# Kernel tuning notes

Hardware: AMD Instinct MI355X
Metric: run time of the kernel (lower is better)

Reference implementation:

```python
import jax, jax.numpy as jnp
import numpy as np

B, D, N, H = 4, 1024, 2048, 16
HD = D // H  # head dim = 64


def rotate_half(x):
    # pairs (x1, x2) -> (-x2, x1), interleaved along last dim
    x1 = x[..., 0::2]
    x2 = x[..., 1::2]
    return jnp.stack((-x2, x1), axis=-1).reshape(x.shape)


def apply_cached_rotary_emb(freqs, t):
    return t * freqs[0] + rotate_half(t) * freqs[1]


def setup_inputs() -> dict:
    key = jax.random.key(0)
    ks = jax.random.split(key, 13)
    s = 1.0 / np.sqrt(D)
    inp = {
        "query": jax.random.normal(ks[0], (B, D, N), jnp.float32),
        "key": jax.random.normal(ks[1], (B, D, N), jnp.float32),
        "value": jax.random.normal(ks[2], (B, D, N), jnp.float32),
        "encoding": jax.random.normal(ks[3], (2, 1, 1, N, HD), jnp.float32),
        "Wq": jax.random.normal(ks[4], (D, D), jnp.float32) * s,
        "bq": jax.random.normal(ks[5], (D,), jnp.float32) * s,
        "Wk": jax.random.normal(ks[6], (D, D), jnp.float32) * s,
        "bk": jax.random.normal(ks[7], (D,), jnp.float32) * s,
        "Wv": jax.random.normal(ks[8], (D, D), jnp.float32) * s,
        "bv": jax.random.normal(ks[9], (D,), jnp.float32) * s,
        "Wm": jax.random.normal(ks[10], (D, D), jnp.float32) * s,
        "bm": jax.random.normal(ks[11], (D,), jnp.float32) * s,
    }
    return inp


def reference(query, key, value, encoding, Wq, bq, Wk, bk, Wv, bv, Wm, bm):
    b, d_model, n = query.shape

    def proj(W, bias, x):  # Conv1d with kernel_size=1 == pointwise matmul
        return jnp.einsum('oi,bin->bon', W, x) + bias[None, :, None]

    # [B, D, N] -> [B, HD, H, N]  (channel split: dim-major, as in .view(B, dim, H, -1))
    q = proj(Wq, bq, query).reshape(b, HD, H, n)
    k = proj(Wk, bk, key).reshape(b, HD, H, n)
    v = proj(Wv, bv, value).reshape(b, HD, H, n)

    # RoPE applied in [B, H, N, HD] layout, then back to [B, HD, H, N]
    q = jnp.transpose(apply_cached_rotary_emb(encoding, jnp.transpose(q, (0, 2, 3, 1))), (0, 3, 1, 2))
    k = jnp.transpose(apply_cached_rotary_emb(encoding, jnp.transpose(k, (0, 2, 3, 1))), (0, 3, 1, 2))

    scores = jnp.einsum('bdhn,bdhm->bhnm', q, k) / np.float32(np.sqrt(HD))
    prob = jax.nn.softmax(scores, axis=-1)
    x = jnp.einsum('bhnm,bdhm->bdhn', prob, v)

    out = jnp.einsum('oi,bin->bon', Wm, x.reshape(b, d_model, n)) + bm[None, :, None]
    return out
```

## Files before the change

### kernel.cpp

```cpp
#include <hip/hip_runtime.h>
#include <hip/hip_bf16.h>

typedef __bf16 bf16;
typedef __bf16 bf16x8 __attribute__((ext_vector_type(8)));
typedef __bf16 bf16x4 __attribute__((ext_vector_type(4)));
typedef float f32x4 __attribute__((ext_vector_type(4)));
typedef unsigned int uint4v __attribute__((ext_vector_type(4)));
typedef unsigned int uint2v __attribute__((ext_vector_type(2)));

#define LOG2E 1.44269504088896340736f

typedef __attribute__((address_space(1))) const unsigned int guint;
typedef __attribute__((address_space(3))) unsigned int luint;

__device__ __forceinline__ void gload_lds16(const bf16* g, bf16* l) {
  __builtin_amdgcn_global_load_lds((guint*)g, (luint*)l, 16, 0, 0);
}

__global__ __launch_bounds__(256) void k_transpose3(const float* __restrict__ q,
                                                    const float* __restrict__ k,
                                                    const float* __restrict__ v,
                                                    bf16* __restrict__ tq,
                                                    bf16* __restrict__ tk,
                                                    bf16* __restrict__ tv) {
  __shared__ bf16 T[64][72];
  const int t = threadIdx.x;
  const int n0 = blockIdx.x * 64;
  const int i0 = blockIdx.y * 64;
  const int z = blockIdx.z;
  const int b = z & 3, which = z >> 2;
  const float* src = (which == 0) ? q : ((which == 1) ? k : v);
  bf16* dst = (which == 0) ? tq : ((which == 1) ? tk : tv);
  const size_t srcb = (size_t)b * 1024 * 2048;
#pragma unroll
  for (int p = 0; p < 2; ++p) {
    int idx = p * 256 + t;
    int row = idx >> 3;
    int seg = idx & 7;
    const float* sp = src + srcb + (size_t)(i0 + row) * 2048 + n0 + seg * 8;
    f32x4 a = *(const f32x4*)sp;
    f32x4 c = *(const f32x4*)(sp + 4);
    bf16x8 o;
#pragma unroll
    for (int e = 0; e < 4; ++e) { o[e] = (bf16)a[e]; o[4 + e] = (bf16)c[e]; }
    *(bf16x8*)&T[row][seg * 8] = o;
  }
  __syncthreads();
  const int j = t >> 2;
  const int iseg = t & 3;
  bf16x8 o0, o1;
#pragma unroll
  for (int e = 0; e < 8; ++e) o0[e] = T[iseg * 16 + e][j];
#pragma unroll
  for (int e = 0; e < 8; ++e) o1[e] = T[iseg * 16 + 8 + e][j];
  bf16* dp = dst + (size_t)b * 2048 * 1024 + (size_t)(n0 + j) * 1024 + i0 + iseg * 16;
  *(bf16x8*)dp = o0;
  *(bf16x8*)(dp + 8) = o1;
}

__global__ __launch_bounds__(256) void k_gemm3(const bf16* __restrict__ Wqb,
                                               const bf16* __restrict__ Wkb,
                                               const bf16* __restrict__ Wvb,
                                               const float* __restrict__ bq,
                                               const float* __restrict__ bk,
                                               const float* __restrict__ bv,
                                               const bf16* __restrict__ tq,
                                               const bf16* __restrict__ tk,
                                               const bf16* __restrict__ tv,
                                               bf16* __restrict__ qp,
                                               bf16* __restrict__ kp,
                                               bf16* __restrict__ vp) {
  const int K = 1024, Nn = 2048;
  const int z = blockIdx.z;
  const int b = z & 3, which = z >> 2;
  const bf16* A = (which == 0) ? Wqb : ((which == 1) ? Wkb : Wvb);
  const bf16* Bt = (which == 0) ? tq : ((which == 1) ? tk : tv);
  const float* bias = (which == 0) ? bq : ((which == 1) ? bk : bv);
  bf16* C = (which == 0) ? qp : ((which == 1) ? kp : vp);

  __shared__ bf16 As[128 * 32];
  __shared__ bf16 Bs[128 * 32];
  const int t = threadIdx.x;
  const int w = t >> 6, l = t & 63, q = l >> 4, li = l & 15;
  const int o0 = blockIdx.y * 128, n0 = blockIdx.x * 128;
  const bf16* Ab = A + (size_t)o0 * K;
  const bf16* Bb = Bt + (size_t)b * Nn * K + (size_t)n0 * K;
  const int wr = (w >> 1) * 64, wc = (w & 1) * 64;
  f32x4 acc[4][4];
#pragma unroll
  for (int i = 0; i < 4; ++i)
#pragma unroll
    for (int j = 0; j < 4; ++j) acc[i][j] = (f32x4){0.f, 0.f, 0.f, 0.f};

  const int sidx0 = w * 64 + l;
  const int srow0 = sidx0 >> 2, sseg0 = (sidx0 & 3) * 8;
  const int sidx1 = 256 + sidx0;
  const int srow1 = sidx1 >> 2, sseg1 = (sidx1 & 3) * 8;
  bf16* ldsA0 = As + (size_t)(w * 64) * 8;
  bf16* ldsA1 = As + (size_t)(256 + w * 64) * 8;
  bf16* ldsB0 = Bs + (size_t)(w * 64) * 8;
  bf16* ldsB1 = Bs + (size_t)(256 + w * 64) * 8;

  for (int k0 = 0; k0 < K; k0 += 32) {
    __syncthreads();
    gload_lds16(Ab + (size_t)srow0 * K + k0 + sseg0, ldsA0);
    gload_lds16(Ab + (size_t)srow1 * K + k0 + sseg1, ldsA1);
    gload_lds16(Bb + (size_t)srow0 * K + k0 + sseg0, ldsB0);
    gload_lds16(Bb + (size_t)srow1 * K + k0 + sseg1, ldsB1);
    __syncthreads();
    bf16x8 af[4], bfr[4];
#pragma unroll
    for (int mt = 0; mt < 4; ++mt) af[mt] = *(const bf16x8*)&As[(wr + mt * 16 + li) * 32 + q * 8];
#pragma unroll
    for (int c = 0; c < 4; ++c) bfr[c] = *(const bf16x8*)&Bs[(wc + c * 16 + li) * 32 + q * 8];
#pragma unroll
    for (int mt = 0; mt < 4; ++mt)
#pragma unroll
      for (int c = 0; c < 4; ++c)
        acc[mt][c] = __builtin_amdgcn_mfma_f32_16x16x32_bf16(af[mt], bfr[c], acc[mt][c], 0, 0, 0);
  }

  bf16* Cb = C + (size_t)b * K * Nn;
#pragma unroll
  for (int mt = 0; mt < 4; ++mt) {
#pragma unroll
    for (int r = 0; r < 4; ++r) {
      int o = o0 + wr + mt * 16 + q * 4 + r;
      float bvv = bias[o];
#pragma unroll
      for (int c = 0; c < 4; ++c) {
        int n = n0 + wc + c * 16 + li;
        Cb[(size_t)o * Nn + n] = (bf16)(acc[mt][c][r] + bvv);
      }
    }
  }
}

template <typename OT>
__global__ __launch_bounds__(256) void k_gemm(const bf16* __restrict__ A,
                                              const bf16* __restrict__ Bt,
                                              const float* __restrict__ bias,
                                              OT* __restrict__ C,
                                              int M, int K, int Nn) {
  __shared__ bf16 As[128 * 32];
  __shared__ bf16 Bs[128 * 32];
  const int t = threadIdx.x;
  const int w = t >> 6, l = t & 63, q = l >> 4, li = l & 15;
  const int o0 = blockIdx.y * 128, n0 = blockIdx.x * 128;
  const int b = blockIdx.z;
  const bf16* Ab = A + (size_t)o0 * K;
  const bf16* Bb = Bt + (size_t)b * Nn * K + (size_t)n0 * K;
  const int wr = (w >> 1) * 64, wc = (w & 1) * 64;
  f32x4 acc[4][4];
#pragma unroll
  for (int i = 0; i < 4; ++i)
#pragma unroll
    for (int j = 0; j < 4; ++j) acc[i][j] = (f32x4){0.f, 0.f, 0.f, 0.f};

  const int sidx0 = w * 64 + l;
  const int srow0 = sidx0 >> 2, sseg0 = (sidx0 & 3) * 8;
  const int sidx1 = 256 + sidx0;
  const int srow1 = sidx1 >> 2, sseg1 = (sidx1 & 3) * 8;
  bf16* ldsA0 = As + (size_t)(w * 64) * 8;
  bf16* ldsA1 = As + (size_t)(256 + w * 64) * 8;
  bf16* ldsB0 = Bs + (size_t)(w * 64) * 8;
  bf16* ldsB1 = Bs + (size_t)(256 + w * 64) * 8;

  for (int k0 = 0; k0 < K; k0 += 32) {
    __syncthreads();
    gload_lds16(Ab + (size_t)srow0 * K + k0 + sseg0, ldsA0);
    gload_lds16(Ab + (size_t)srow1 * K + k0 + sseg1, ldsA1);
    gload_lds16(Bb + (size_t)srow0 * K + k0 + sseg0, ldsB0);
    gload_lds16(Bb + (size_t)srow1 * K + k0 + sseg1, ldsB1);
    __syncthreads();
    bf16x8 af[4], bfr[4];
#pragma unroll
    for (int mt = 0; mt < 4; ++mt) af[mt] = *(const bf16x8*)&As[(wr + mt * 16 + li) * 32 + q * 8];
#pragma unroll
    for (int c = 0; c < 4; ++c) bfr[c] = *(const bf16x8*)&Bs[(wc + c * 16 + li) * 32 + q * 8];
#pragma unroll
    for (int mt = 0; mt < 4; ++mt)
#pragma unroll
      for (int c = 0; c < 4; ++c)
        acc[mt][c] = __builtin_amdgcn_mfma_f32_16x16x32_bf16(af[mt], bfr[c], acc[mt][c], 0, 0, 0);
  }

  OT* Cb = C + (size_t)b * M * Nn;
#pragma unroll
  for (int mt = 0; mt < 4; ++mt) {
#pragma unroll
    for (int r = 0; r < 4; ++r) {
      int o = o0 + wr + mt * 16 + q * 4 + r;
      float bv = bias[o];
#pragma unroll
      for (int c = 0; c < 4; ++c) {
        int n = n0 + wc + c * 16 + li;
        Cb[(size_t)o * Nn + n] = (OT)(acc[mt][c][r] + bv);
      }
    }
  }
}

__global__ __launch_bounds__(256) void k_rope2(const bf16* __restrict__ qp,
                                               const bf16* __restrict__ kp,
                                               const float* __restrict__ enc,
                                               bf16* __restrict__ qa,
                                               bf16* __restrict__ ka) {
  __shared__ bf16 T[64][72];
  const int t = threadIdx.x;
  const int n0 = blockIdx.x * 64;
  const int h = blockIdx.y;
  const int z = blockIdx.z;
  const int b = z & 3, which = z >> 2;
  const bf16* src = which ? kp : qp;
  bf16* dst = which ? ka : qa;
  const float oscale = which ? 1.0f : 0.125f * LOG2E;
#pragma unroll
  for (int p = 0; p < 2; ++p) {
    int idx = p * 256 + t;
    int hd = idx >> 3;
    int seg = idx & 7;
    *(bf16x8*)&T[hd][seg * 8] =
        *(const bf16x8*)(src + (size_t)(b * 1024 + hd * 16 + h) * 2048 + n0 + seg * 8);
  }
  __syncthreads();
  const int j = t >> 2;
  const int hd0 = (t & 3) * 16;
  const int n = n0 + j;
  const float* e0 = enc + (size_t)n * 64 + hd0;
  const float* e1 = enc + (size_t)2048 * 64 + (size_t)n * 64 + hd0;
  bf16x8 o0, o1;
#pragma unroll
  for (int i = 0; i < 8; ++i) {
    int e = 2 * i;
    float t0 = (float)T[hd0 + e][j];
    float t1 = (float)T[hd0 + e + 1][j];
    float f00 = e0[e], f01 = e0[e + 1];
    float f10 = e1[e], f11 = e1[e + 1];
    float r0 = (t0 * f00 - t1 * f10) * oscale;
    float r1 = (t1 * f01 + t0 * f11) * oscale;
    if (i < 4) { o0[e & 7] = (bf16)r0; o0[(e & 7) + 1] = (bf16)r1; }
    else       { o1[e & 7] = (bf16)r0; o1[(e & 7) + 1] = (bf16)r1; }
  }
  bf16* dp = dst + ((size_t)(b * 16 + h) * 2048 + n) * 64 + hd0;
  *(bf16x8*)dp = o0;
  *(bf16x8*)(dp + 8) = o1;
}

__global__ __launch_bounds__(256, 4) void k_attn(const bf16* __restrict__ qa,
                                                 const bf16* __restrict__ ka,
                                                 const bf16* __restrict__ vp,
                                                 bf16* __restrict__ xo) {
  __shared__ bf16 Ks[64 * 72];
  __shared__ bf16 Vs[64 * 72];
  const int t = threadIdx.x;
  const int w = t >> 6, l = t & 63, q = l >> 4, li = l & 15;
  const int n0 = blockIdx.x * 128, h = blockIdx.y, b = blockIdx.z;
  const bool oddrow = ((t >> 4) & 1) != 0;
  const bf16* Qb = qa + (size_t)(b * 16 + h) * 2048 * 64;
  const bf16* Kb = ka + (size_t)(b * 16 + h) * 2048 * 64;
  const bf16* Vb = vp + (size_t)b * 1024 * 2048 + (size_t)h * 2048;

  const int r0 = t >> 3, s0 = (t & 7) * 8;
  const int r1 = (256 + t) >> 3, s1 = (t & 7) * 8;

  bf16x8 qf[2][2];
#pragma unroll
  for (int bt = 0; bt < 2; ++bt)
#pragma unroll
    for (int kk = 0; kk < 2; ++kk)
      qf[bt][kk] = *(const bf16x8*)(Qb + (size_t)(n0 + w * 32 + bt * 16 + li) * 64 + kk * 32 + q * 8);

  bf16x8 onef;
#pragma unroll
  for (int e = 0; e < 8; ++e) onef[e] = (bf16)1.0f;

  f32x4 acc[4][2];
#pragma unroll
  for (int i = 0; i < 4; ++i)
#pragma unroll
    for (int j = 0; j < 2; ++j) acc[i][j] = (f32x4){0.f, 0.f, 0.f, 0.f};
  f32x4 accl[2] = {(f32x4){0.f, 0.f, 0.f, 0.f}, (f32x4){0.f, 0.f, 0.f, 0.f}};

  bf16x8 kr0, kr1, vr0, vr1;
  kr0 = *(const bf16x8*)(Kb + (size_t)r0 * 64 + s0);
  kr1 = *(const bf16x8*)(Kb + (size_t)r1 * 64 + s1);
  vr0 = *(const bf16x8*)(Vb + (size_t)r0 * 32768 + s0);
  vr1 = *(const bf16x8*)(Vb + (size_t)r1 * 32768 + s1);
  *(bf16x8*)&Ks[r0 * 72 + s0] = kr0;
  *(bf16x8*)&Ks[r1 * 72 + s1] = kr1;
  *(bf16x8*)&Vs[r0 * 72 + s0] = vr0;
  *(bf16x8*)&Vs[r1 * 72 + s1] = vr1;
  __syncthreads();

  for (int m0 = 0; m0 < 2048; m0 += 64) {
    const int mn = (m0 + 64 < 2048) ? m0 + 64 : m0;
    kr0 = *(const bf16x8*)(Kb + (size_t)(mn + r0) * 64 + s0);
    kr1 = *(const bf16x8*)(Kb + (size_t)(mn + r1) * 64 + s1);
    vr0 = *(const bf16x8*)(Vb + (size_t)r0 * 32768 + mn + s0);
    vr1 = *(const bf16x8*)(Vb + (size_t)r1 * 32768 + mn + s1);

    f32x4 sacc[4][2];
#pragma unroll
    for (int mt = 0; mt < 4; ++mt)
#pragma unroll
      for (int bt = 0; bt < 2; ++bt) sacc[mt][bt] = (f32x4){0.f, 0.f, 0.f, 0.f};
#pragma unroll
    for (int kk = 0; kk < 2; ++kk) {
#pragma unroll
      for (int mt = 0; mt < 4; ++mt) {
        bf16x8 af = *(const bf16x8*)&Ks[(mt * 16 + li) * 72 + kk * 32 + q * 8];
#pragma unroll
        for (int bt = 0; bt < 2; ++bt)
          sacc[mt][bt] = __builtin_amdgcn_mfma_f32_16x16x32_bf16(af, qf[bt][kk], sacc[mt][bt], 0, 0, 0);
      }
    }

    unsigned pk32[2][4][2];
#pragma unroll
    for (int mt = 0; mt < 4; ++mt)
#pragma unroll
      for (int bt = 0; bt < 2; ++bt) {
        bf16x4 pk;
#pragma unroll
        for (int r = 0; r < 4; ++r) pk[r] = (bf16)__builtin_amdgcn_exp2f(sacc[mt][bt][r]);
        uint2v pu = __builtin_bit_cast(uint2v, pk);
        pk32[bt][mt][0] = pu[0];
        pk32[bt][mt][1] = pu[1];
      }

#pragma unroll
    for (int kk = 0; kk < 2; ++kk) {
      bf16x8 pf[2];
#pragma unroll
      for (int bt = 0; bt < 2; ++bt) {
        uint4v du;
#pragma unroll
        for (int hh = 0; hh < 2; ++hh) {
          unsigned p0 = pk32[bt][2 * kk + 0][hh];
          unsigned p1 = pk32[bt][2 * kk + 1][hh];
          uint2v ab = __builtin_amdgcn_permlane32_swap(p0, p1, false, false);
          unsigned A = ab[0];
          unsigned Bv = ab[1];
          unsigned swzA = (unsigned)__builtin_amdgcn_ds_swizzle((int)A, 0x401F);
          unsigned swzB = (unsigned)__builtin_amdgcn_ds_swizzle((int)Bv, 0x401F);
          du[hh]     = oddrow ? swzB : A;
          du[2 + hh] = oddrow ? Bv : swzA;
        }
        pf[bt] = __builtin_bit_cast(bf16x8, du);
        accl[bt] = __builtin_amdgcn_mfma_f32_16x16x32_bf16(onef, pf[bt], accl[bt], 0, 0, 0);
      }
#pragma unroll
      for (int hdt = 0; hdt < 4; ++hdt) {
        bf16x8 vf = *(const bf16x8*)&Vs[(hdt * 16 + li) * 72 + kk * 32 + q * 8];
#pragma unroll
        for (int bt = 0; bt < 2; ++bt)
          acc[hdt][bt] = __builtin_amdgcn_mfma_f32_16x16x32_bf16(vf, pf[bt], acc[hdt][bt], 0, 0, 0);
      }
    }

    __syncthreads();
    *(bf16x8*)&Ks[r0 * 72 + s0] = kr0;
    *(bf16x8*)&Ks[r1 * 72 + s1] = kr1;
    *(bf16x8*)&Vs[r0 * 72 + s0] = vr0;
    *(bf16x8*)&Vs[r1 * 72 + s1] = vr1;
    __syncthreads();
  }

  float inv[2] = {1.0f / accl[0][0], 1.0f / accl[1][0]};

  bf16* xb = xo + (size_t)b * 2048 * 1024 + (size_t)h * 64;
#pragma unroll
  for (int hdt = 0; hdt < 4; ++hdt)
#pragma unroll
    for (int bt = 0; bt < 2; ++bt) {
      int n = n0 + w * 32 + bt * 16 + li;
      bf16x4 o;
#pragma unroll
      for (int r = 0; r < 4; ++r) o[r] = (bf16)(acc[hdt][bt][r] * inv[bt]);
      *(bf16x4*)(xb + (size_t)n * 1024 + hdt * 16 + q * 4) = o;
    }
}

__global__ __launch_bounds__(256) void k_prepw(const float* __restrict__ Wq,
                                               const float* __restrict__ Wk,
                                               const float* __restrict__ Wv,
                                               const float* __restrict__ Wm,
                                               bf16* __restrict__ oq,
                                               bf16* __restrict__ ok,
                                               bf16* __restrict__ ov,
                                               bf16* __restrict__ om) {
  const int which = blockIdx.y;
  if (which < 3) {
    const float* s = (which == 0) ? Wq : ((which == 1) ? Wk : Wv);
    bf16* d = (which == 0) ? oq : ((which == 1) ? ok : ov);
    int idx = (blockIdx.x * 256 + threadIdx.x) * 4;
    f32x4 a = *(const f32x4*)(s + idx);
    bf16x4 o;
#pragma unroll
    for (int e = 0; e < 4; ++e) o[e] = (bf16)a[e];
    *(bf16x4*)(d + idx) = o;
  } else {
#pragma unroll
    for (int p = 0; p < 4; ++p) {
      int idx = (blockIdx.x * 4 + p) * 256 + threadIdx.x;
      int o = idx >> 10, j = idx & 1023;
      int hd = j & 63, hh = j >> 6;
      om[idx] = (bf16)Wm[((size_t)o << 10) + (size_t)(hd * 16 + hh)];
    }
  }
}

extern "C" void kernel_launch(void* const* d_in, const int* in_sizes, int n_in,
                              void* d_out, int out_size, void* d_ws, size_t ws_size,
                              hipStream_t stream) {
  const float* query = (const float*)d_in[0];
  const float* key   = (const float*)d_in[1];
  const float* value = (const float*)d_in[2];
  const float* enc   = (const float*)d_in[3];
  const float* Wq = (const float*)d_in[4];  const float* bq = (const float*)d_in[5];
  const float* Wk = (const float*)d_in[6];  const float* bk = (const float*)d_in[7];
  const float* Wv = (const float*)d_in[8];  const float* bv = (const float*)d_in[9];
  const float* Wm = (const float*)d_in[10]; const float* bm = (const float*)d_in[11];

  char* ws = (char*)d_ws;
  const size_t SZ = (size_t)4 * 2048 * 1024 * 2;
  const size_t WZ = (size_t)1024 * 1024 * 2;
  bf16* bufA = (bf16*)(ws + 0 * SZ);
  bf16* bufB = (bf16*)(ws + 1 * SZ);
  bf16* bufC = (bf16*)(ws + 2 * SZ);
  bf16* bufD = (bf16*)(ws + 3 * SZ);
  bf16* Wqb  = (bf16*)(ws + 4 * SZ + 0 * WZ);
  bf16* Wkb  = (bf16*)(ws + 4 * SZ + 1 * WZ);
  bf16* Wvb  = (bf16*)(ws + 4 * SZ + 2 * WZ);
  bf16* Wmp  = (bf16*)(ws + 4 * SZ + 3 * WZ);
  bf16* vt   = (bf16*)d_out;
  bf16* vpd  = (bf16*)d_out + (size_t)4 * 2048 * 1024;

  dim3 blk(256);
  k_prepw<<<dim3(1024, 4), blk, 0, stream>>>(Wq, Wk, Wv, Wm, Wqb, Wkb, Wvb, Wmp);
  k_transpose3<<<dim3(32, 16, 12), blk, 0, stream>>>(query, key, value, bufA, bufB, vt);
  k_gemm3<<<dim3(16, 8, 12), blk, 0, stream>>>(Wqb, Wkb, Wvb, bq, bk, bv,
                                               bufA, bufB, vt, bufC, bufD, vpd);
  k_rope2<<<dim3(32, 16, 8), blk, 0, stream>>>(bufC, bufD, enc, bufA, bufB);
  k_attn<<<dim3(16, 16, 4), blk, 0, stream>>>(bufA, bufB, vpd, bufC);
  k_gemm<float><<<dim3(16, 8, 4), blk, 0, stream>>>(Wmp, bufC, bm, (float*)d_out, 1024, 1024, 2048);
}
```

Before: 362.3 us.

## Double-buffer K/V LDS tiles in attention and remap block order for XCD locality

The attention kernel now keeps two LDS buffers for the K and V tiles. The next tile is written into the idle buffer, so each iteration needs one barrier instead of two. All three GEMM/attention kernels also remap the linear block index so that consecutive blocks that share operands land on the same XCD (dsp&7 chiplet interleave), which should improve L2 reuse. Doubling LDS raises per-block shared memory to about 36KB. That could limit occupancy under the 4-blocks-per-CU launch bound.

New measurement: 375.3 us. 1.04x slower.

```diff
diff --git a/kernel.cpp b/kernel.cpp
--- a/kernel.cpp
+++ b/kernel.cpp
@@ -71,8 +71,10 @@
                                                bf16* __restrict__ kp,
                                                bf16* __restrict__ vp) {
   const int K = 1024, Nn = 2048;
-  const int z = blockIdx.z;
-  const int b = z & 3, which = z >> 2;
+  const int dsp = blockIdx.x + 16 * (blockIdx.y + 8 * blockIdx.z);
+  const int wfi = (dsp & 7) * 192 + (dsp >> 3);
+  const int bx = wfi & 15, by = (wfi >> 4) & 7, bz = wfi >> 7;
+  const int b = bz & 3, which = bz >> 2;
   const bf16* A = (which == 0) ? Wqb : ((which == 1) ? Wkb : Wvb);
   const bf16* Bt = (which == 0) ? tq : ((which == 1) ? tk : tv);
   const float* bias = (which == 0) ? bq : ((which == 1) ? bk : bv);
@@ -82,7 +84,7 @@
   __shared__ bf16 Bs[128 * 32];
   const int t = threadIdx.x;
   const int w = t >> 6, l = t & 63, q = l >> 4, li = l & 15;
-  const int o0 = blockIdx.y * 128, n0 = blockIdx.x * 128;
+  const int o0 = by * 128, n0 = bx * 128;
   const bf16* Ab = A + (size_t)o0 * K;
   const bf16* Bb = Bt + (size_t)b * Nn * K + (size_t)n0 * K;
   const int wr = (w >> 1) * 64, wc = (w & 1) * 64;
@@ -146,8 +148,11 @@
   __shared__ bf16 Bs[128 * 32];
   const int t = threadIdx.x;
   const int w = t >> 6, l = t & 63, q = l >> 4, li = l & 15;
-  const int o0 = blockIdx.y * 128, n0 = blockIdx.x * 128;
-  const int b = blockIdx.z;
+  const int dsp = blockIdx.x + 16 * (blockIdx.y + 8 * blockIdx.z);
+  const int wfi = (dsp & 7) * 64 + (dsp >> 3);
+  const int bx = wfi & 15, by = (wfi >> 4) & 7, bz = wfi >> 7;
+  const int o0 = by * 128, n0 = bx * 128;
+  const int b = bz;
   const bf16* Ab = A + (size_t)o0 * K;
   const bf16* Bb = Bt + (size_t)b * Nn * K + (size_t)n0 * K;
   const int wr = (w >> 1) * 64, wc = (w & 1) * 64;
@@ -251,11 +256,13 @@
                                                  const bf16* __restrict__ ka,
                                                  const bf16* __restrict__ vp,
                                                  bf16* __restrict__ xo) {
-  __shared__ bf16 Ks[64 * 72];
-  __shared__ bf16 Vs[64 * 72];
+  __shared__ bf16 Ks2[2][64 * 72];
+  __shared__ bf16 Vs2[2][64 * 72];
   const int t = threadIdx.x;
   const int w = t >> 6, l = t & 63, q = l >> 4, li = l & 15;
-  const int n0 = blockIdx.x * 128, h = blockIdx.y, b = blockIdx.z;
+  const int dsp = blockIdx.x + 16 * (blockIdx.y + 16 * blockIdx.z);
+  const int wfi = (dsp & 7) * 128 + (dsp >> 3);
+  const int n0 = (wfi & 15) * 128, h = (wfi >> 4) & 15, b = wfi >> 8;
   const bool oddrow = ((t >> 4) & 1) != 0;
   const bf16* Qb = qa + (size_t)(b * 16 + h) * 2048 * 64;
   const bf16* Kb = ka + (size_t)(b * 16 + h) * 2048 * 64;
@@ -287,18 +294,24 @@
   kr1 = *(const bf16x8*)(Kb + (size_t)r1 * 64 + s1);
   vr0 = *(const bf16x8*)(Vb + (size_t)r0 * 32768 + s0);
   vr1 = *(const bf16x8*)(Vb + (size_t)r1 * 32768 + s1);
-  *(bf16x8*)&Ks[r0 * 72 + s0] = kr0;
-  *(bf16x8*)&Ks[r1 * 72 + s1] = kr1;
-  *(bf16x8*)&Vs[r0 * 72 + s0] = vr0;
-  *(bf16x8*)&Vs[r1 * 72 + s1] = vr1;
+  *(bf16x8*)&Ks2[0][r0 * 72 + s0] = kr0;
+  *(bf16x8*)&Ks2[0][r1 * 72 + s1] = kr1;
+  *(bf16x8*)&Vs2[0][r0 * 72 + s0] = vr0;
+  *(bf16x8*)&Vs2[0][r1 * 72 + s1] = vr1;
   __syncthreads();
 
+  int cur = 0;
   for (int m0 = 0; m0 < 2048; m0 += 64) {
-    const int mn = (m0 + 64 < 2048) ? m0 + 64 : m0;
-    kr0 = *(const bf16x8*)(Kb + (size_t)(mn + r0) * 64 + s0);
-    kr1 = *(const bf16x8*)(Kb + (size_t)(mn + r1) * 64 + s1);
-    vr0 = *(const bf16x8*)(Vb + (size_t)r0 * 32768 + mn + s0);
-    vr1 = *(const bf16x8*)(Vb + (size_t)r1 * 32768 + mn + s1);
+    const bf16* ks = Ks2[cur];
+    const bf16* vs = Vs2[cur];
+    const bool more = (m0 + 64) < 2048;
+    if (more) {
+      const int mn = m0 + 64;
+      kr0 = *(const bf16x8*)(Kb + (size_t)(mn + r0) * 64 + s0);
+      kr1 = *(const bf16x8*)(Kb + (size_t)(mn + r1) * 64 + s1);
+      vr0 = *(const bf16x8*)(Vb + (size_t)r0 * 32768 + mn + s0);
+      vr1 = *(const bf16x8*)(Vb + (size_t)r1 * 32768 + mn + s1);
+    }
 
     f32x4 sacc[4][2];
 #pragma unroll
@@ -309,7 +322,7 @@
     for (int kk = 0; kk < 2; ++kk) {
 #pragma unroll
       for (int mt = 0; mt < 4; ++mt) {
-        bf16x8 af = *(const bf16x8*)&Ks[(mt * 16 + li) * 72 + kk * 32 + q * 8];
+        bf16x8 af = *(const bf16x8*)&ks[(mt * 16 + li) * 72 + kk * 32 + q * 8];
 #pragma unroll
         for (int bt = 0; bt < 2; ++bt)
           sacc[mt][bt] = __builtin_amdgcn_mfma_f32_16x16x32_bf16(af, qf[bt][kk], sacc[mt][bt], 0, 0, 0);
@@ -352,19 +365,23 @@
       }
 #pragma unroll
       for (int hdt = 0; hdt < 4; ++hdt) {
-        bf16x8 vf = *(const bf16x8*)&Vs[(hdt * 16 + li) * 72 + kk * 32 + q * 8];
+        bf16x8 vf = *(const bf16x8*)&vs[(hdt * 16 + li) * 72 + kk * 32 + q * 8];
 #pragma unroll
         for (int bt = 0; bt < 2; ++bt)
           acc[hdt][bt] = __builtin_amdgcn_mfma_f32_16x16x32_bf16(vf, pf[bt], acc[hdt][bt], 0, 0, 0);
       }
     }
 
+    if (more) {
+      bf16* kd = Ks2[cur ^ 1];
+      bf16* vd = Vs2[cur ^ 1];
+      *(bf16x8*)&kd[r0 * 72 + s0] = kr0;
+      *(bf16x8*)&kd[r1 * 72 + s1] = kr1;
+      *(bf16x8*)&vd[r0 * 72 + s0] = vr0;
+      *(bf16x8*)&vd[r1 * 72 + s1] = vr1;
+    }
     __syncthreads();
-    *(bf16x8*)&Ks[r0 * 72 + s0] = kr0;
-    *(bf16x8*)&Ks[r1 * 72 + s1] = kr1;
-    *(bf16x8*)&Vs[r0 * 72 + s0] = vr0;
-    *(bf16x8*)&Vs[r1 * 72 + s1] = vr1;
-    __syncthreads();
+    cur ^= 1;
   }
 
   float inv[2] = {1.0f / accl[0][0], 1.0f / accl[1][0]};
```
